# Kernel optimization log

Hardware: AMD Instinct MI355X
Metric: run time of the kernel (lower is better)

Reference implementation:

```python
import jax, jax.numpy as jnp
import numpy as np
from jax import lax

NPOINT = 1024
NSAMPLE = 32
RADIUS = 0.2
EPS = 1e-5  # BatchNorm eps (torch default)
MLP = [64, 64, 128]
IN_CHANNEL = 6  # 3 (relative xyz) + 3 (point features)


def setup_inputs() -> dict:
    key = jax.random.key(0)
    ks = jax.random.split(key, 2 + len(MLP))
    B, N, D = 16, 4096, 3
    inp = {
        "xyz": jax.random.uniform(ks[0], (B, N, 3), jnp.float32),
        "points": jax.random.normal(ks[1], (B, N, D), jnp.float32),
    }
    last = IN_CHANNEL
    for i, co in enumerate(MLP):
        inp[f"w{i}"] = jax.random.normal(ks[2 + i], (co, last), jnp.float32) * (1.0 / np.sqrt(last))
        inp[f"b{i}"] = jnp.zeros((co,), jnp.float32)
        inp[f"gamma{i}"] = jnp.ones((co,), jnp.float32)
        inp[f"beta{i}"] = jnp.zeros((co,), jnp.float32)
        last = co
    return inp


def index_points(points, idx):
    # points: [B, N, C]; idx: [B, S] or [B, S, K] -> [B, S, C] or [B, S, K, C]
    B, C = points.shape[0], points.shape[-1]
    flat = idx.reshape(B, -1)
    out = jnp.take_along_axis(points, flat[:, :, None], axis=1)
    return out.reshape(idx.shape + (C,))


def farthest_point_sample(xyz, npoint):
    # Deterministic FPS (start index 0 per batch); torch version uses a random start.
    B, N, _ = xyz.shape

    def step(carry, _):
        dist, far = carry
        centroid = jnp.take_along_axis(xyz, far[:, None, None], axis=1)  # [B,1,3]
        d = jnp.sum((xyz - centroid) ** 2, axis=-1)  # [B,N]
        dist = jnp.minimum(dist, d)
        return (dist, jnp.argmax(dist, axis=-1).astype(jnp.int32)), far

    init = (jnp.full((B, N), 1e10, dtype=xyz.dtype), jnp.zeros((B,), jnp.int32))
    _, fars = lax.scan(step, init, None, length=npoint)  # [npoint, B]
    return jnp.transpose(fars)  # [B, npoint]


def square_distance(src, dst):
    # [B,N,3] x [B,M,3] -> [B,N,M] squared distances
    d = -2.0 * jnp.einsum('bnc,bmc->bnm', src, dst)
    d = d + jnp.sum(src ** 2, -1)[:, :, None]
    d = d + jnp.sum(dst ** 2, -1)[:, None, :]
    return d


def query_ball_point(radius, nsample, xyz, new_xyz):
    B, N, _ = xyz.shape
    sqr = square_distance(new_xyz, xyz)  # [B,S,N]
    idx = jnp.broadcast_to(jnp.arange(N, dtype=jnp.int32), sqr.shape)
    idx = jnp.where(sqr > radius ** 2, N, idx)
    idx = jnp.sort(idx, axis=-1)[:, :, :nsample]  # [B,S,nsample]
    first = idx[:, :, :1]
    return jnp.where(idx == N, first, idx)


def reference(xyz, points,
              w0, b0, gamma0, beta0,
              w1, b1, gamma1, beta1,
              w2, b2, gamma2, beta2):
    fps_idx = farthest_point_sample(xyz, NPOINT)          # [B,S]
    new_xyz = index_points(xyz, fps_idx)                  # [B,S,3]
    idx = query_ball_point(RADIUS, NSAMPLE, xyz, new_xyz)  # [B,S,K]
    grouped_xyz = index_points(xyz, idx) - new_xyz[:, :, None, :]  # [B,S,K,3]
    grouped_pts = index_points(points, idx)               # [B,S,K,D]
    x = jnp.concatenate([grouped_xyz, grouped_pts], axis=-1)  # [B,S,K,3+D]

    for (w, b, g, be) in [(w0, b0, gamma0, beta0),
                          (w1, b1, gamma1, beta1),
                          (w2, b2, gamma2, beta2)]:
        x = jnp.einsum('bskc,oc->bsko', x, w) + b  # 1x1 Conv2d
        mean = x.mean(axis=(0, 1, 2))
        var = x.var(axis=(0, 1, 2))  # biased, matches BN training-mode normalization
        x = jax.nn.relu(g * (x - mean) * lax.rsqrt(var + EPS) + be)

    new_points = x.max(axis=2)  # max-pool over the K neighbor dim -> [B,S,mlp[-1]]
    return new_xyz, new_points
```

## Files before the change

kernel.cpp:

```cpp
#include <hip/hip_runtime.h>
#include <stdint.h>

#define B_ 16
#define N_ 4096
#define S_ 1024
#define K_ 32
#define NQ_ (B_*S_)
#define NPIX_ (NQ_*K_)
#define OUTNP_ (NQ_*3)
#define EPS_ 1e-5f


#define DPPMAX64(x, CTRL) do { \
  unsigned _lo = (unsigned)(x); unsigned _hi = (unsigned)((x)>>32); \
  unsigned _plo = (unsigned)__builtin_amdgcn_update_dpp((int)_lo,(int)_lo,(CTRL),0xF,0xF,false); \
  unsigned _phi = (unsigned)__builtin_amdgcn_update_dpp((int)_hi,(int)_hi,(CTRL),0xF,0xF,false); \
  unsigned long long _p = (((unsigned long long)_phi)<<32)|_plo; \
  if (_p > (x)) (x) = _p; \
} while(0)

#define DPPMAXF(r, CTRL) do { \
  float _t = __int_as_float(__builtin_amdgcn_update_dpp(__float_as_int(r),__float_as_int(r),(CTRL),0xF,0xF,false)); \
  (r) = fmaxf((r), _t); \
} while(0)

__global__ __launch_bounds__(512) void k_fps(const float* __restrict__ xyz,
                                             float* __restrict__ out,
                                             float* __restrict__ nx) {
  const int b = blockIdx.x;
  const int t = threadIdx.x;
  const int lane = t & 63, wid = t >> 6;
  __shared__ int SX[N_], SY[N_], SZ[N_];
  __shared__ unsigned long long kbuf[2][8];
  const float* xb = xyz + (size_t)b * N_ * 3;
  for (int j = t; j < N_; j += 512) {
    SX[j] = (int)(xb[j*3+0] * 536870912.0f);
    SY[j] = (int)(xb[j*3+1] * 536870912.0f);
    SZ[j] = (int)(xb[j*3+2] * 536870912.0f);
  }
  __syncthreads();
  int PX[8], PY[8], PZ[8];
  unsigned long long key[8];
#pragma unroll
  for (int i = 0; i < 8; ++i) {
    const int j = t*8 + i;
    PX[i] = SX[j]; PY[i] = SY[j]; PZ[i] = SZ[j];
    key[i] = ~0ull;
  }
  int far = 0;
  for (int it = 0; it < S_; ++it) {
    const int cx = SX[far], cy = SY[far], cz = SZ[far];
    if (t == 0) {
      const int o = (b*S_ + it)*3;
      const float fx = (float)cx * 1.862645149230957e-9f;
      const float fy = (float)cy * 1.862645149230957e-9f;
      const float fz = (float)cz * 1.862645149230957e-9f;
      out[o] = fx; out[o+1] = fy; out[o+2] = fz;
      nx[o]  = fx; nx[o+1]  = fy; nx[o+2]  = fz;
    }
    if (it == S_-1) break;
    unsigned long long best = 0;
#pragma unroll
    for (int i = 0; i < 8; ++i) {
      const int dx = PX[i]-cx, dy = PY[i]-cy, dz = PZ[i]-cz;
      unsigned long long nk = (unsigned long long)(unsigned)(4095 - (t*8 + i));
      nk += (unsigned long long)((long long)dx*dx);
      nk += (unsigned long long)((long long)dy*dy);
      nk += (unsigned long long)((long long)dz*dz);
      if (nk < key[i]) key[i] = nk;
      if (key[i] > best) best = key[i];
    }
    DPPMAX64(best, 0x111);
    DPPMAX64(best, 0x112);
    DPPMAX64(best, 0x114);
    DPPMAX64(best, 0x118);
    DPPMAX64(best, 0x142);
    DPPMAX64(best, 0x143);
    if (lane == 63) kbuf[it & 1][wid] = best;
    __syncthreads();
    unsigned long long g = kbuf[it & 1][lane & 7];
    DPPMAX64(g, 0x111); DPPMAX64(g, 0x112); DPPMAX64(g, 0x114);
    far = 4095 - (__builtin_amdgcn_readlane((int)(unsigned)g, 7) & 4095);
  }
}

__global__ __launch_bounds__(256) void k_ball(const float* __restrict__ xyz,
                                              const float* __restrict__ nx,
                                              int* __restrict__ idx,
                                              const float* __restrict__ w0,
                                              const float* __restrict__ w1,
                                              const float* __restrict__ w2,
                                              float* __restrict__ w0t,
                                              float* __restrict__ w1t,
                                              float* __restrict__ w2t) {
  if (blockIdx.x == NQ_/4) {
    const int t = threadIdx.x;
    for (int i = t; i < 64*6; i += 256)  { int o = i/6,  c = i%6;  w0t[c*64  + o] = w0[i]; }
    for (int i = t; i < 64*64; i += 256) { int o = i>>6, c = i&63; w1t[c*64  + o] = w1[i]; }
    for (int i = t; i < 128*64; i += 256){ int o = i>>6, c = i&63; w2t[c*128 + o] = w2[i]; }
    return;
  }
  const int lane = threadIdx.x & 63;
  const int q = blockIdx.x * 4 + (threadIdx.x >> 6);
  const int b = q >> 10;
  const float* xb = xyz + (size_t)b * N_ * 3;
  const double qx = (double)nx[q*3+0], qy = (double)nx[q*3+1], qz = (double)nx[q*3+2];
  const double qq = qx*qx + qy*qy + qz*qz;
  const double r2 = 0.2 * 0.2;
  int found = 0, first_j = 0;
  bool have_first = false;
  for (int c = 0; c < N_/64; ++c) {
    const int j = c*64 + lane;
    const double px = (double)xb[j*3+0], py = (double)xb[j*3+1], pz = (double)xb[j*3+2];
    const double dot = px*qx + py*qy + pz*qz;
    const double pp  = px*px + py*py + pz*pz;
    const double d   = qq + pp - 2.0*dot;
    const bool hit = (d <= r2);
    const unsigned long long mask = __ballot(hit);
    if (!have_first && mask) { first_j = c*64 + (__ffsll(mask) - 1); have_first = true; }
    const int pos = found + (int)__popcll(mask & ((1ull << lane) - 1ull));
    if (hit && pos < K_) idx[q*K_ + pos] = j;
    found += (int)__popcll(mask);
    if (found >= K_) break;
  }
  const int cnt = found < K_ ? found : K_;
  if (lane >= cnt && lane < K_) idx[q*K_ + lane] = first_j;
}

__global__ __launch_bounds__(256) void k_momw(const float* __restrict__ xyz,
                                              const float* __restrict__ points,
                                              const float* __restrict__ nx,
                                              const int* __restrict__ idx,
                                              float* __restrict__ momp) {
  const int tid = blockIdx.x * blockDim.x + threadIdx.x;
  float m[6] = {0,0,0,0,0,0};
  float M2[21];
#pragma unroll
  for (int u = 0; u < 21; ++u) M2[u] = 0.0f;
  int js[8], qs[8];
#pragma unroll
  for (int r = 0; r < 8; ++r) {
    const int pix = tid + (r << 16);
    js[r] = idx[pix]; qs[r] = pix >> 5;
  }
#pragma unroll
  for (int r = 0; r < 8; ++r) {
    const int b = qs[r] >> 10;
    const float* xp = xyz    + (size_t)(b*N_ + js[r])*3;
    const float* pq = points + (size_t)(b*N_ + js[r])*3;
    const float* nq = nx + qs[r]*3;
    float g[6];
    g[0] = xp[0]-nq[0]; g[1] = xp[1]-nq[1]; g[2] = xp[2]-nq[2];
    g[3] = pq[0]; g[4] = pq[1]; g[5] = pq[2];
#pragma unroll
    for (int i = 0; i < 6; ++i) m[i] += g[i];
    int u = 0;
#pragma unroll
    for (int i = 0; i < 6; ++i)
#pragma unroll
      for (int jj = i; jj < 6; ++jj) { M2[u] = fmaf(g[i], g[jj], M2[u]); ++u; }
  }
#pragma unroll
  for (int i = 0; i < 6; ++i)
#pragma unroll
    for (int s = 1; s < 64; s <<= 1) m[i] += __shfl_xor(m[i], s);
#pragma unroll
  for (int u = 0; u < 21; ++u)
#pragma unroll
    for (int s = 1; s < 64; s <<= 1) M2[u] += __shfl_xor(M2[u], s);
  if ((threadIdx.x & 63) == 0) {
    const int w = blockIdx.x * 4 + (threadIdx.x >> 6);
    float* dst = momp + w*32;
#pragma unroll
    for (int i = 0; i < 6; ++i) dst[i] = m[i];
#pragma unroll
    for (int u = 0; u < 21; ++u) dst[6+u] = M2[u];
  }
}

__global__ void k_fin0r(const float* __restrict__ momp,
                        const float* __restrict__ w0, const float* __restrict__ b0,
                        const float* __restrict__ g0, const float* __restrict__ be0,
                        float* __restrict__ pr) {
  __shared__ float part[8][32];
  __shared__ float red[32];
  const int t = threadIdx.x;
  const int c = t & 31, p = t >> 5;
  float a = 0.f;
  for (int w = p; w < 1024; w += 8) a += momp[w*32 + c];
  part[p][c] = a;
  __syncthreads();
  if (t < 32) {
    float s = 0.f;
#pragma unroll
    for (int pp = 0; pp < 8; ++pp) s += part[pp][c];
    red[c] = s;
  }
  __syncthreads();
  if (t < 64) {
    const float inv = 1.0f / (float)NPIX_;
    float m1[6];
#pragma unroll
    for (int i = 0; i < 6; ++i) m1[i] = red[i] * inv;
    float M2[6][6];
    int u = 0;
#pragma unroll
    for (int i = 0; i < 6; ++i)
#pragma unroll
      for (int jj = i; jj < 6; ++jj) { float v = red[6+u]*inv; M2[i][jj] = v; M2[jj][i] = v; ++u; }
    float w[6];
#pragma unroll
    for (int i = 0; i < 6; ++i) w[i] = w0[t*6+i];
    float ml = 0.0f;
#pragma unroll
    for (int i = 0; i < 6; ++i) ml += w[i]*m1[i];
    float e2 = 0.0f;
#pragma unroll
    for (int i = 0; i < 6; ++i)
#pragma unroll
      for (int jj = 0; jj < 6; ++jj) e2 += w[i]*w[jj]*M2[i][jj];
    const float var = e2 - ml*ml;
    const float mean = ml + b0[t];
    const float sc = g0[t] * rsqrtf(var + EPS_);
    pr[t] = sc; pr[64+t] = be0[t] - mean*sc;
  }
}

__global__ void k_fin1r(const float* __restrict__ s1p,
                        const float* __restrict__ g1, const float* __restrict__ be1,
                        float* __restrict__ pr) {
  __shared__ float pa[4][64], pb[4][64];
  const int t = threadIdx.x;
  const int c = t & 63, p = t >> 6;
  const int wq = c >> 4, u = c & 15;
  float sa = 0.f, sb = 0.f;
  for (int blk = p; blk < 1024; blk += 4) {
    const int w = blk*4 + wq;
    sa += s1p[w*32 + u];
    sb += s1p[w*32 + 16 + u];
  }
  pa[p][c] = sa; pb[p][c] = sb;
  __syncthreads();
  if (t < 64) {
    const float A  = pa[0][t]+pa[1][t]+pa[2][t]+pa[3][t];
    const float Bq = pb[0][t]+pb[1][t]+pb[2][t]+pb[3][t];
    const float inv = 1.0f / (float)NPIX_;
    const float mean = A*inv;
    const float var = Bq*inv - mean*mean;
    const float sc = g1[t] * rsqrtf(var + EPS_);
    pr[128+t] = sc; pr[192+t] = be1[t] - mean*sc;
  }
}

__global__ void k_fin2r(const float* __restrict__ s2p,
                        const float* __restrict__ g2, const float* __restrict__ be2,
                        float* __restrict__ pr) {
  __shared__ float pa[2][128], pb[2][128];
  const int t = threadIdx.x;
  const int c = t & 127, p = t >> 7;
  const int wq = c >> 5, u = c & 31;
  float sa = 0.f, sb = 0.f;
  for (int blk = p; blk < 1024; blk += 2) {
    const int w = blk*4 + wq;
    sa += s2p[w*64 + u];
    sb += s2p[w*64 + 32 + u];
  }
  pa[p][c] = sa; pb[p][c] = sb;
  __syncthreads();
  if (t < 128) {
    const float A  = pa[0][t]+pa[1][t];
    const float Bq = pb[0][t]+pb[1][t];
    const float inv = 1.0f / (float)NPIX_;
    const float mean = A*inv;
    const float var = Bq*inv - mean*mean;
    const float sc = g2[t] * rsqrtf(var + EPS_);
    pr[256+t] = sc; pr[384+t] = be2[t] - mean*sc;
  }
}

__global__ void k_mom(const float* __restrict__ xyz, const float* __restrict__ points,
                      const float* __restrict__ nx, const int* __restrict__ idx,
                      float* __restrict__ st) {
  const int tid = blockIdx.x * blockDim.x + threadIdx.x;
  float m[6] = {0,0,0,0,0,0};
  float M2[21];
#pragma unroll
  for (int u = 0; u < 21; ++u) M2[u] = 0.0f;
  int js[8], qs[8];
#pragma unroll
  for (int r = 0; r < 8; ++r) { const int pix = tid + (r << 16); js[r] = idx[pix]; qs[r] = pix >> 5; }
#pragma unroll
  for (int r = 0; r < 8; ++r) {
    const int b = qs[r] >> 10;
    const float* xp = xyz    + (size_t)(b*N_ + js[r])*3;
    const float* pq = points + (size_t)(b*N_ + js[r])*3;
    const float* nq = nx + qs[r]*3;
    float g[6];
    g[0] = xp[0]-nq[0]; g[1] = xp[1]-nq[1]; g[2] = xp[2]-nq[2];
    g[3] = pq[0]; g[4] = pq[1]; g[5] = pq[2];
#pragma unroll
    for (int i = 0; i < 6; ++i) m[i] += g[i];
    int u = 0;
#pragma unroll
    for (int i = 0; i < 6; ++i)
#pragma unroll
      for (int jj = i; jj < 6; ++jj) { M2[u] = fmaf(g[i], g[jj], M2[u]); ++u; }
  }
#pragma unroll
  for (int i = 0; i < 6; ++i)
#pragma unroll
    for (int s = 1; s < 64; s <<= 1) m[i] += __shfl_xor(m[i], s);
#pragma unroll
  for (int u = 0; u < 21; ++u)
#pragma unroll
    for (int s = 1; s < 64; s <<= 1) M2[u] += __shfl_xor(M2[u], s);
  if ((threadIdx.x & 63) == 0) {
#pragma unroll
    for (int i = 0; i < 6; ++i) atomicAdd(&st[i], m[i]);
#pragma unroll
    for (int u = 0; u < 21; ++u) atomicAdd(&st[6+u], M2[u]);
  }
}

__global__ void k_fin0(const float* __restrict__ w0, const float* __restrict__ b0,
                       const float* __restrict__ g0, const float* __restrict__ be0,
                       const float* __restrict__ st, float* __restrict__ pr) {
  const int c = threadIdx.x;
  const float inv = 1.0f / (float)NPIX_;
  float m1[6];
#pragma unroll
  for (int i = 0; i < 6; ++i) m1[i] = st[i] * inv;
  float M2[6][6];
  int u = 0;
#pragma unroll
  for (int i = 0; i < 6; ++i)
#pragma unroll
    for (int jj = i; jj < 6; ++jj) { float v = st[6+u]*inv; M2[i][jj] = v; M2[jj][i] = v; ++u; }
  float w[6];
#pragma unroll
  for (int i = 0; i < 6; ++i) w[i] = w0[c*6+i];
  float ml = 0.0f;
#pragma unroll
  for (int i = 0; i < 6; ++i) ml += w[i]*m1[i];
  float e2 = 0.0f;
#pragma unroll
  for (int i = 0; i < 6; ++i)
#pragma unroll
    for (int jj = 0; jj < 6; ++jj) e2 += w[i]*w[jj]*M2[i][jj];
  const float var = e2 - ml*ml;
  const float mean = ml + b0[c];
  const float sc = g0[c] * rsqrtf(var + EPS_);
  pr[c] = sc; pr[64+c] = be0[c] - mean*sc;
}

__global__ void k_fin(const float* __restrict__ gam, const float* __restrict__ bet,
                      const float* __restrict__ ssum, const float* __restrict__ ssq,
                      float* __restrict__ psc, float* __restrict__ psh) {
  const int c = threadIdx.x;
  const float inv = 1.0f / (float)NPIX_;
  const float mean = ssum[c]*inv;
  const float var = ssq[c]*inv - mean*mean;
  const float sc = gam[c] * rsqrtf(var + EPS_);
  psc[c] = sc; psh[c] = bet[c] - mean*sc;
}

__global__ __launch_bounds__(256) void k_s1(
    const float* __restrict__ xyz, const float* __restrict__ points,
    const float* __restrict__ nx, const int* __restrict__ idx,
    const float* __restrict__ w0t, const float* __restrict__ w1t,
    const float* __restrict__ b0, const float* __restrict__ b1,
    const float* __restrict__ pr, float* __restrict__ s1p,
    float* __restrict__ a1)
{
  __shared__ float a0T[64][64];
  const int tid = threadIdx.x;
  const int lane = tid & 63;
  const int wid = __builtin_amdgcn_readfirstlane(tid >> 6);
  const int c0 = wid * 16;
  float b0r[16], b1r[16], p0s[16], p0h[16];
#pragma unroll
  for (int u = 0; u < 16; ++u) {
    b0r[u] = b0[c0+u]; b1r[u] = b1[c0+u];
    p0s[u] = pr[c0+u]; p0h[u] = pr[64+c0+u];
  }
  float s1a[16], s1b[16];
#pragma unroll
  for (int u = 0; u < 16; ++u) { s1a[u] = 0.0f; s1b[u] = 0.0f; }

  for (int tile = blockIdx.x; tile < NQ_/2; tile += gridDim.x) {
    const int q = tile*2 + (lane >> 5);
    const int k = lane & 31;
    const int b = q >> 10;
    const int j = idx[q*K_ + k];
    const float* xp = xyz    + (size_t)(b*N_ + j)*3;
    const float* pp = points + (size_t)(b*N_ + j)*3;
    const float* nq = nx + q*3;
    float g[6];
    g[0] = xp[0]-nq[0]; g[1] = xp[1]-nq[1]; g[2] = xp[2]-nq[2];
    g[3] = pp[0];       g[4] = pp[1];       g[5] = pp[2];
    float acc[16];
#pragma unroll
    for (int u = 0; u < 16; ++u) acc[u] = b0r[u];
#pragma unroll
    for (int i = 0; i < 6; ++i) {
      const float* w = w0t + i*64 + c0;
#pragma unroll
      for (int u = 0; u < 16; ++u) acc[u] = fmaf(w[u], g[i], acc[u]);
    }
#pragma unroll
    for (int u = 0; u < 16; ++u)
      a0T[c0+u][lane] = fmaxf(fmaf(p0s[u], acc[u], p0h[u]), 0.0f);
    __syncthreads();
#pragma unroll
    for (int u = 0; u < 16; ++u) acc[u] = b1r[u];
#pragma unroll 8
    for (int ci = 0; ci < 64; ++ci) {
      const float av = a0T[ci][lane];
      const float* w = w1t + ci*64 + c0;
#pragma unroll
      for (int u = 0; u < 16; ++u) acc[u] = fmaf(w[u], av, acc[u]);
    }
    const int pix = tile*64 + lane;
#pragma unroll
    for (int u = 0; u < 16; ++u) {
      s1a[u] += acc[u]; s1b[u] = fmaf(acc[u], acc[u], s1b[u]);
      a1[(size_t)(c0+u)*NPIX_ + pix] = acc[u];
    }
    __syncthreads();
  }
#pragma unroll
  for (int u = 0; u < 16; ++u) {
    float a = s1a[u], bq = s1b[u];
#pragma unroll
    for (int s = 1; s < 64; s <<= 1) { a += __shfl_xor(a, s); bq += __shfl_xor(bq, s); }
    s1a[u] = a; s1b[u] = bq;
  }
  if (lane == 0) {
    float* dst = s1p + (blockIdx.x*4 + wid)*32;
#pragma unroll
    for (int u = 0; u < 16; ++u) { dst[u] = s1a[u]; dst[16+u] = s1b[u]; }
  }
}

__global__ __launch_bounds__(256) void k_s2(
    const float* __restrict__ a1, const float* __restrict__ w2t,
    const float* __restrict__ b2, const float* __restrict__ g2,
    const float* __restrict__ pr, float* __restrict__ s2p,
    float* __restrict__ pooled)
{
  __shared__ float a1T[64][64];
  const int tid = threadIdx.x;
  const int lane = tid & 63;
  const int wid = __builtin_amdgcn_readfirstlane(tid >> 6);
  const int cl = wid * 16;
  const int c20 = wid * 32;
  float p1s[16], p1h[16], b2r[32];
  bool g2p[32];
#pragma unroll
  for (int u = 0; u < 16; ++u) { p1s[u] = pr[128+cl+u]; p1h[u] = pr[192+cl+u]; }
#pragma unroll
  for (int u = 0; u < 32; ++u) { b2r[u] = b2[c20+u]; g2p[u] = (g2[c20+u] >= 0.0f); }
  float s2a[32], s2b[32];
#pragma unroll
  for (int u = 0; u < 32; ++u) { s2a[u] = 0.0f; s2b[u] = 0.0f; }

  for (int tile = blockIdx.x; tile < NQ_/2; tile += gridDim.x) {
    const int pixb = tile*64;
#pragma unroll
    for (int u = 0; u < 16; ++u) {
      const float v = a1[(size_t)(cl+u)*NPIX_ + pixb + lane];
      a1T[cl+u][lane] = fmaxf(fmaf(p1s[u], v, p1h[u]), 0.0f);
    }
    __syncthreads();
    float acc2[32];
#pragma unroll
    for (int u = 0; u < 32; ++u) acc2[u] = b2r[u];
#pragma unroll 8
    for (int ci = 0; ci < 64; ++ci) {
      const float av = a1T[ci][lane];
      const float* w = w2t + ci*128 + c20;
#pragma unroll
      for (int u = 0; u < 32; ++u) acc2[u] = fmaf(w[u], av, acc2[u]);
    }
    const int q = tile*2 + (lane >> 5);
#pragma unroll
    for (int u = 0; u < 32; ++u) {
      s2a[u] += acc2[u]; s2b[u] = fmaf(acc2[u], acc2[u], s2b[u]);
      float r = g2p[u] ? acc2[u] : -acc2[u];
      DPPMAXF(r, 0xB1);
      DPPMAXF(r, 0x4E);
      DPPMAXF(r, 0x141);
      DPPMAXF(r, 0x140);
      DPPMAXF(r, 0x142);
      if ((lane & 31) == 31) pooled[q*128 + c20 + u] = g2p[u] ? r : -r;
    }
    __syncthreads();
  }
#pragma unroll
  for (int u = 0; u < 32; ++u) {
    float a = s2a[u], bq = s2b[u];
#pragma unroll
    for (int s = 1; s < 64; s <<= 1) { a += __shfl_xor(a, s); bq += __shfl_xor(bq, s); }
    s2a[u] = a; s2b[u] = bq;
  }
  if (lane == 0) {
    float* dst = s2p + (blockIdx.x*4 + wid)*64;
#pragma unroll
    for (int u = 0; u < 32; ++u) { dst[u] = s2a[u]; dst[32+u] = s2b[u]; }
  }
}

__global__ __launch_bounds__(256) void k_s3(const float* __restrict__ pooled,
                                            const float* __restrict__ pr,
                                            float* __restrict__ out) {
  const int g = blockIdx.x * 256 + threadIdx.x;
  const int c = g & 127;
  const float y = fmaf(pr[256+c], pooled[g], pr[384+c]);
  out[OUTNP_ + g] = fmaxf(y, 0.0f);
}

template<int STAGE>
__global__ __launch_bounds__(256) void k_stage(
    const float* __restrict__ xyz, const float* __restrict__ points,
    const float* __restrict__ nx, const int* __restrict__ idx,
    const float* __restrict__ w0t, const float* __restrict__ w1t,
    const float* __restrict__ w2t,
    const float* __restrict__ b0, const float* __restrict__ b1,
    const float* __restrict__ b2,
    const float* __restrict__ pr, float* __restrict__ st,
    float* __restrict__ out)
{
  __shared__ float gT[6][64];
  __shared__ float a0T[64][64];
  __shared__ float a1T[64][64];
  const int tid = threadIdx.x;
  const int lane = tid & 63;
  const int wid = __builtin_amdgcn_readfirstlane(tid >> 6);
  const int c0 = wid * 16;
  const int c20 = wid * 32;

  float s1a[16], s1b[16], s2a[32], s2b[32];
  if (STAGE == 1) {
#pragma unroll
    for (int u = 0; u < 16; ++u) { s1a[u] = 0.0f; s1b[u] = 0.0f; }
  }
  if (STAGE == 2) {
#pragma unroll
    for (int u = 0; u < 32; ++u) { s2a[u] = 0.0f; s2b[u] = 0.0f; }
  }

  for (int tile = blockIdx.x; tile < NQ_/2; tile += gridDim.x) {
    const int q = tile*2 + (lane >> 5);
    const int k = lane & 31;
    if (wid == 0) {
      const int b = q >> 10;
      const int j = idx[q*K_ + k];
      const float* xp = xyz    + (size_t)(b*N_ + j)*3;
      const float* pp = points + (size_t)(b*N_ + j)*3;
      const float* nq = nx + q*3;
      gT[0][lane] = xp[0]-nq[0]; gT[1][lane] = xp[1]-nq[1]; gT[2][lane] = xp[2]-nq[2];
      gT[3][lane] = pp[0];       gT[4][lane] = pp[1];       gT[5][lane] = pp[2];
    }
    __syncthreads();
    float acc[16];
#pragma unroll
    for (int u = 0; u < 16; ++u) acc[u] = b0[c0+u];
#pragma unroll
    for (int i = 0; i < 6; ++i) {
      const float av = gT[i][lane];
      const float* w = w0t + i*64 + c0;
#pragma unroll
      for (int u = 0; u < 16; ++u) acc[u] = fmaf(w[u], av, acc[u]);
    }
#pragma unroll
    for (int u = 0; u < 16; ++u) {
      const float a = fmaf(pr[c0+u], acc[u], pr[64+c0+u]);
      a0T[c0+u][lane] = fmaxf(a, 0.0f);
    }
    __syncthreads();
#pragma unroll
    for (int u = 0; u < 16; ++u) acc[u] = b1[c0+u];
#pragma unroll 8
    for (int ci = 0; ci < 64; ++ci) {
      const float av = a0T[ci][lane];
      const float* w = w1t + ci*64 + c0;
#pragma unroll
      for (int u = 0; u < 16; ++u) acc[u] = fmaf(w[u], av, acc[u]);
    }
    if (STAGE == 1) {
#pragma unroll
      for (int u = 0; u < 16; ++u) { s1a[u] += acc[u]; s1b[u] = fmaf(acc[u], acc[u], s1b[u]); }
    } else {
#pragma unroll
      for (int u = 0; u < 16; ++u) {
        const float a = fmaf(pr[128+c0+u], acc[u], pr[192+c0+u]);
        a1T[c0+u][lane] = fmaxf(a, 0.0f);
      }
      __syncthreads();
      float acc2[32];
#pragma unroll
      for (int u = 0; u < 32; ++u) acc2[u] = b2[c20+u];
#pragma unroll 8
      for (int ci = 0; ci < 64; ++ci) {
        const float av = a1T[ci][lane];
        const float* w = w2t + ci*128 + c20;
#pragma unroll
        for (int u = 0; u < 32; ++u) acc2[u] = fmaf(w[u], av, acc2[u]);
      }
      if (STAGE == 2) {
#pragma unroll
        for (int u = 0; u < 32; ++u) { s2a[u] += acc2[u]; s2b[u] = fmaf(acc2[u], acc2[u], s2b[u]); }
      } else {
#pragma unroll
        for (int u = 0; u < 32; ++u) {
          float y = fmaf(pr[256+c20+u], acc2[u], pr[384+c20+u]);
#pragma unroll
          for (int s = 1; s < 32; s <<= 1) y = fmaxf(y, __shfl_xor(y, s));
          if ((lane & 31) == 0) out[OUTNP_ + q*128 + c20 + u] = fmaxf(y, 0.0f);
        }
      }
    }
    __syncthreads();
  }
  if (STAGE == 1) {
#pragma unroll
    for (int u = 0; u < 16; ++u) {
      float a = s1a[u], bq = s1b[u];
#pragma unroll
      for (int s = 1; s < 64; s <<= 1) { a += __shfl_xor(a, s); bq += __shfl_xor(bq, s); }
      if (lane == 0) { atomicAdd(&st[32 + c0+u], a); atomicAdd(&st[96 + c0+u], bq); }
    }
  }
  if (STAGE == 2) {
#pragma unroll
    for (int u = 0; u < 32; ++u) {
      float a = s2a[u], bq = s2b[u];
#pragma unroll
      for (int s = 1; s < 64; s <<= 1) { a += __shfl_xor(a, s); bq += __shfl_xor(bq, s); }
      if (lane == 0) { atomicAdd(&st[160 + c20+u], a); atomicAdd(&st[288 + c20+u], bq); }
    }
  }
}

extern "C" void kernel_launch(void* const* d_in, const int* in_sizes, int n_in,
                              void* d_out, int out_size, void* d_ws, size_t ws_size,
                              hipStream_t stream) {
  const float* xyz    = (const float*)d_in[0];
  const float* points = (const float*)d_in[1];
  const float* w0  = (const float*)d_in[2];
  const float* b0  = (const float*)d_in[3];
  const float* g0  = (const float*)d_in[4];
  const float* be0 = (const float*)d_in[5];
  const float* w1  = (const float*)d_in[6];
  const float* b1  = (const float*)d_in[7];
  const float* g1  = (const float*)d_in[8];
  const float* be1 = (const float*)d_in[9];
  const float* w2  = (const float*)d_in[10];
  const float* b2  = (const float*)d_in[11];
  const float* g2  = (const float*)d_in[12];
  const float* be2 = (const float*)d_in[13];
  float* out = (float*)d_out;
  float* ws  = (float*)d_ws;

  float* nx  = ws;
  int*   idx = (int*)(ws + 49152);
  float* w0t = ws + 573440;
  float* w1t = ws + 573824;
  float* w2t = ws + 577920;
  float* st  = ws + 586112;
  float* pr  = ws + 586624;
  float* pooled = ws + 587264;
  float* a1  = ws + 2684928;
  float* momp = pooled;
  float* s1p  = pooled + 32768;
  float* s2p  = (float*)(ws + 49152);

  const size_t need = (size_t)(2684928 + 33554432) * sizeof(float);
  const bool big = ws_size >= need;

  k_fps<<<B_, 512, 0, stream>>>(xyz, out, nx);
  k_ball<<<NQ_/4 + 1, 256, 0, stream>>>(xyz, nx, idx, w0, w1, w2, w0t, w1t, w2t);
  if (big) {
    k_momw<<<256, 256, 0, stream>>>(xyz, points, nx, idx, momp);
    k_fin0r<<<1, 256, 0, stream>>>(momp, w0, b0, g0, be0, pr);
    k_s1<<<1024, 256, 0, stream>>>(xyz, points, nx, idx, w0t, w1t, b0, b1, pr, s1p, a1);
    k_fin1r<<<1, 256, 0, stream>>>(s1p, g1, be1, pr);
    k_s2<<<1024, 256, 0, stream>>>(a1, w2t, b2, g2, pr, s2p, pooled);
    k_fin2r<<<1, 256, 0, stream>>>(s2p, g2, be2, pr);
    k_s3<<<NPIX_*4/256, 256, 0, stream>>>(pooled, pr, out);
  } else {
    hipMemsetAsync(st, 0, 512*sizeof(float), stream);
    k_mom<<<256, 256, 0, stream>>>(xyz, points, nx, idx, st);
    k_fin0<<<1, 64, 0, stream>>>(w0, b0, g0, be0, st, pr);
    k_stage<1><<<1024, 256, 0, stream>>>(xyz, points, nx, idx, w0t, w1t, w2t, b0, b1, b2, pr, st, out);
    k_fin<<<1, 64, 0, stream>>>(g1, be1, st+32, st+96, pr+128, pr+192);
    k_stage<2><<<1024, 256, 0, stream>>>(xyz, points, nx, idx, w0t, w1t, w2t, b0, b1, b2, pr, st, out);
    k_fin<<<1, 128, 0, stream>>>(g2, be2, st+160, st+288, pr+256, pr+384);
    k_stage<3><<<1024, 256, 0, stream>>>(xyz, points, nx, idx, w0t, w1t, w2t, b0, b1, b2, pr, st, out);
  }
}
```

Baseline: 1.255 ms.

## Pack FPS coords into int4 LDS, defer centroid writes, pool in-place to output

The FPS kernel now stores quantized xyz as one int4 per point in LDS, so each centroid fetch is a single vector load instead of three scalar loads. Each thread records the selected indices for its two iterations and writes all centroids in one batch after the loop, which takes the per-iteration global stores by thread 0 off the serial critical path. Separately, the pooled max output is written directly into the output buffer, and the final BN/ReLU pass runs in place, removing one intermediate buffer read. The LDS footprint grows by a third because of the padding lane.

```diff
diff --git a/kernel.cpp b/kernel.cpp
--- a/kernel.cpp
+++ b/kernel.cpp
@@ -30,35 +30,30 @@
   const int b = blockIdx.x;
   const int t = threadIdx.x;
   const int lane = t & 63, wid = t >> 6;
-  __shared__ int SX[N_], SY[N_], SZ[N_];
+  __shared__ int4 SXYZ[N_];
   __shared__ unsigned long long kbuf[2][8];
   const float* xb = xyz + (size_t)b * N_ * 3;
   for (int j = t; j < N_; j += 512) {
-    SX[j] = (int)(xb[j*3+0] * 536870912.0f);
-    SY[j] = (int)(xb[j*3+1] * 536870912.0f);
-    SZ[j] = (int)(xb[j*3+2] * 536870912.0f);
+    SXYZ[j] = make_int4((int)(xb[j*3+0] * 536870912.0f),
+                        (int)(xb[j*3+1] * 536870912.0f),
+                        (int)(xb[j*3+2] * 536870912.0f), 0);
   }
   __syncthreads();
   int PX[8], PY[8], PZ[8];
   unsigned long long key[8];
 #pragma unroll
   for (int i = 0; i < 8; ++i) {
-    const int j = t*8 + i;
-    PX[i] = SX[j]; PY[i] = SY[j]; PZ[i] = SZ[j];
+    const int4 p = SXYZ[t*8 + i];
+    PX[i] = p.x; PY[i] = p.y; PZ[i] = p.z;
     key[i] = ~0ull;
   }
-  int far = 0;
+  int far = 0, farA = 0, farB = 0;
   for (int it = 0; it < S_; ++it) {
-    const int cx = SX[far], cy = SY[far], cz = SZ[far];
-    if (t == 0) {
-      const int o = (b*S_ + it)*3;
-      const float fx = (float)cx * 1.862645149230957e-9f;
-      const float fy = (float)cy * 1.862645149230957e-9f;
-      const float fz = (float)cz * 1.862645149230957e-9f;
-      out[o] = fx; out[o+1] = fy; out[o+2] = fz;
-      nx[o]  = fx; nx[o+1]  = fy; nx[o+2]  = fz;
-    }
+    if (it == t)       farA = far;
+    if (it == t + 512) farB = far;
     if (it == S_-1) break;
+    const int4 c4 = SXYZ[far];
+    const int cx = c4.x, cy = c4.y, cz = c4.z;
     unsigned long long best = 0;
 #pragma unroll
     for (int i = 0; i < 8; ++i) {
@@ -81,6 +76,17 @@
     unsigned long long g = kbuf[it & 1][lane & 7];
     DPPMAX64(g, 0x111); DPPMAX64(g, 0x112); DPPMAX64(g, 0x114);
     far = 4095 - (__builtin_amdgcn_readlane((int)(unsigned)g, 7) & 4095);
+  }
+  {
+    const int4 a = SXYZ[farA];
+    const int4 c = SXYZ[farB];
+    const float s = 1.862645149230957e-9f;
+    const int oA = (b*S_ + t)*3;
+    const int oB = (b*S_ + t + 512)*3;
+    out[oA] = (float)a.x*s; out[oA+1] = (float)a.y*s; out[oA+2] = (float)a.z*s;
+    nx[oA]  = (float)a.x*s; nx[oA+1]  = (float)a.y*s; nx[oA+2]  = (float)a.z*s;
+    out[oB] = (float)c.x*s; out[oB+1] = (float)c.y*s; out[oB+2] = (float)c.z*s;
+    nx[oB]  = (float)c.x*s; nx[oB+1]  = (float)c.y*s; nx[oB+2]  = (float)c.z*s;
   }
 }
 
@@ -510,13 +516,12 @@
   }
 }
 
-__global__ __launch_bounds__(256) void k_s3(const float* __restrict__ pooled,
-                                            const float* __restrict__ pr,
-                                            float* __restrict__ out) {
+__global__ __launch_bounds__(256) void k_s3(const float* __restrict__ pr,
+                                            float* __restrict__ outnp) {
   const int g = blockIdx.x * 256 + threadIdx.x;
   const int c = g & 127;
-  const float y = fmaf(pr[256+c], pooled[g], pr[384+c]);
-  out[OUTNP_ + g] = fmaxf(y, 0.0f);
+  const float y = fmaf(pr[256+c], outnp[g], pr[384+c]);
+  outnp[g] = fmaxf(y, 0.0f);
 }
 
 template<int STAGE>
@@ -669,11 +674,11 @@
   float* w2t = ws + 577920;
   float* st  = ws + 586112;
   float* pr  = ws + 586624;
-  float* pooled = ws + 587264;
   float* a1  = ws + 2684928;
-  float* momp = pooled;
-  float* s1p  = pooled + 32768;
+  float* momp = ws + 587264;
+  float* s1p  = ws + 587264 + 32768;
   float* s2p  = (float*)(ws + 49152);
+  float* pooled = out + OUTNP_;
 
   const size_t need = (size_t)(2684928 + 33554432) * sizeof(float);
   const bool big = ws_size >= need;
@@ -687,7 +692,7 @@
     k_fin1r<<<1, 256, 0, stream>>>(s1p, g1, be1, pr);
     k_s2<<<1024, 256, 0, stream>>>(a1, w2t, b2, g2, pr, s2p, pooled);
     k_fin2r<<<1, 256, 0, stream>>>(s2p, g2, be2, pr);
-    k_s3<<<NPIX_*4/256, 256, 0, stream>>>(pooled, pr, out);
+    k_s3<<<NPIX_*4/256, 256, 0, stream>>>(pr, pooled);
   } else {
     hipMemsetAsync(st, 0, 512*sizeof(float), stream);
     k_mom<<<256, 256, 0, stream>>>(xyz, points, nx, idx, st);
```

New measurement: 1.295 ms. 3.2% more time.
